# Performance work log

Measured on AMD Instinct MI355X. Metric: run time of the kernel, lower is better.

Reference implementation:

```python
import jax, jax.numpy as jnp
import numpy as np

V, D, L, H, FF, B, S = 32000, 2048, 4, 16, 8192, 2, 2048
DH = D // H
PRUNE_LAYERS = (1, 2)   # layers with an attached pruning module
KEEP_RATIO = 0.5        # keep_ratio arg of forward_prefill_with_pruning


def _rms(x, w, eps=1e-6):
    return x * w * jax.lax.rsqrt(jnp.mean(x * x, -1, keepdims=True) + eps)


def _rope(x):
    # x: [B,H,s,DH]; position_ids = arange(s), recomputed after every pruning step
    s = x.shape[2]
    half = DH // 2
    inv = 1.0 / (10000.0 ** (jnp.arange(half, dtype=jnp.float32) / half))
    ang = jnp.arange(s, dtype=jnp.float32)[:, None] * inv  # [s, half]
    cos, sin = jnp.cos(ang), jnp.sin(ang)
    x1, x2 = x[..., :half], x[..., half:]
    return jnp.concatenate([x1 * cos - x2 * sin, x1 * sin + x2 * cos], -1)


def _block(h, mask, wq, wk, wv, wo, wg, wu, wd, ln1, ln2):
    b, s, _ = h.shape
    hn = _rms(h, ln1)
    q = _rope((hn @ wq).reshape(b, s, H, DH).transpose(0, 2, 1, 3))
    k = _rope((hn @ wk).reshape(b, s, H, DH).transpose(0, 2, 1, 3))
    v = (hn @ wv).reshape(b, s, H, DH).transpose(0, 2, 1, 3)
    att = jnp.einsum('bhqd,bhkd->bhqk', q, k) / np.float32(np.sqrt(DH))
    allowed = jnp.tril(jnp.ones((s, s), bool)) & (mask[:, None, None, :] > 0)
    att = jnp.where(allowed, att, jnp.float32(-1e9))
    o = jnp.einsum('bhqk,bhkd->bhqd', jax.nn.softmax(att, -1), v)
    h = h + o.transpose(0, 2, 1, 3).reshape(b, s, D) @ wo
    hn = _rms(h, ln2)
    h = h + (jax.nn.silu(hn @ wg) * (hn @ wu)) @ wd
    return h


def _forward(input_ids, attention_mask, embed, wq, wk, wv, wo, wg, wu, wd, ln1, ln2, lnf, lm_head, scorer):
    h = embed[input_ids]        # [B,S,D]
    mask = attention_mask
    for i in range(L):
        if i in PRUNE_LAYERS:
            pi = PRUNE_LAYERS.index(i)
            # pruning module: Linear(D->2); keep score = logits[..., 0]
            sc = jnp.einsum('bsd,cd->bsc', h, scorer[pi])[..., 0]
            kk = max(1, int(h.shape[1] * KEEP_RATIO))      # static under jit
            _, idx = jax.lax.top_k(sc, kk)
            idx = jnp.sort(idx, -1)                        # sorted kept indices
            h = jnp.take_along_axis(h, idx[..., None], axis=1)
            mask = jnp.take_along_axis(mask, idx, axis=1)
        h = _block(h, mask, wq[i], wk[i], wv[i], wo[i], wg[i], wu[i], wd[i], ln1[i], ln2[i])
    return _rms(h, lnf) @ lm_head   # logits [B, S_pruned, V]


def setup_inputs() -> dict:
    key = jax.random.key(0)
    ks = jax.random.split(key, 12)
    g = lambda k, shape: jax.random.normal(k, shape, jnp.float32) * 0.02
    return {
        'input_ids': jax.random.randint(ks[0], (B, S), 0, V, jnp.int32),
        'attention_mask': jnp.ones((B, S), jnp.int32),
        'embed': g(ks[1], (V, D)),
        'wq': g(ks[2], (L, D, D)),
        'wk': g(ks[3], (L, D, D)),
        'wv': g(ks[4], (L, D, D)),
        'wo': g(ks[5], (L, D, D)),
        'wg': g(ks[6], (L, D, FF)),
        'wu': g(ks[7], (L, D, FF)),
        'wd': g(ks[8], (L, FF, D)),
        'ln1': jnp.ones((L, D), jnp.float32),
        'ln2': jnp.ones((L, D), jnp.float32),
        'lnf': jnp.ones((D,), jnp.float32),
        'lm_head': g(ks[9], (D, V)),
        'scorer': g(ks[10], (len(PRUNE_LAYERS), 2, D)),
    }


def reference(input_ids, attention_mask, embed, wq, wk, wv, wo, wg, wu, wd, ln1, ln2, lnf, lm_head, scorer):
    return _forward(input_ids, attention_mask, embed, wq, wk, wv, wo, wg, wu, wd, ln1, ln2, lnf, lm_head, scorer)
```

## Files before the change

kernel.cpp:

```cpp
#include <hip/hip_runtime.h>
#include <math.h>


#define DD 2048
#define HH 16
#define DHH 128
#define FFF 8192
#define BBATCH 2
#define SSEQ 2048
#define VV 32000
#define LLAYERS 4

typedef float4 f4;
typedef __attribute__((ext_vector_type(8))) short short8;
typedef __attribute__((ext_vector_type(4))) float f32x4;
typedef unsigned short u16;

__device__ inline u16 bf16rne(float x) {
    unsigned u = __float_as_uint(x);
    unsigned r = (u + 0x7FFFu + ((u >> 16) & 1u)) >> 16;
    return (u16)r;
}
__device__ inline float bf16tof(u16 h) {
    return __uint_as_float(((unsigned)h) << 16);
}

__device__ __forceinline__ void gload16(const u16* g, u16* l) {
    __builtin_amdgcn_global_load_lds(
        (const __attribute__((address_space(1))) unsigned int*)g,
        (__attribute__((address_space(3))) unsigned int*)l, 16, 0, 0);
}

#define BARRIER() do { asm volatile("" ::: "memory"); \
    __builtin_amdgcn_s_barrier(); asm volatile("" ::: "memory"); } while (0)

__device__ __forceinline__ void xcd_swz(int& bx, int& by) {
    int gy = gridDim.y;
    int nwg = gridDim.x * gy;
    int orig = bx * gy + by;
    int q = nwg >> 3, r = nwg & 7;
    int xcd = orig & 7, loc = orig >> 3;
    int swz = (xcd < r ? xcd * (q + 1) : r * (q + 1) + (xcd - r) * q) + loc;
    bx = swz / gy;
    by = swz % gy;
}

__global__ void k_embed(const int* __restrict__ ids, const float* __restrict__ emb,
                        float* __restrict__ out) {
    int row = blockIdx.x;
    int id  = ids[row];
    const f4* src = (const f4*)(emb + (size_t)id * DD);
    f4*       dst = (f4*)(out + (size_t)row * DD);
    for (int i = threadIdx.x; i < DD / 4; i += blockDim.x) dst[i] = src[i];
}

__global__ void k_copy_int(const int* __restrict__ src, int* __restrict__ dst, int n) {
    int i = blockIdx.x * blockDim.x + threadIdx.x;
    if (i < n) dst[i] = src[i];
}

__global__ void k_addN(float* __restrict__ H, const float* __restrict__ P,
                       long len, int nparts) {
    long i = (long)blockIdx.x * 256 + threadIdx.x;
    if (i >= len / 4) return;
    f4 h = ((f4*)H)[i];
    for (int z = 0; z < nparts; z++) {
        f4 p = ((const f4*)(P + (size_t)z * len))[i];
        h.x += p.x; h.y += p.y; h.z += p.z; h.w += p.w;
    }
    ((f4*)H)[i] = h;
}

__global__ __launch_bounds__(256) void k_rmsnorm_cvt(const float* __restrict__ x,
                                                     const float* __restrict__ w,
                                                     u16* __restrict__ OH,
                                                     u16* __restrict__ OL) {
    int row = blockIdx.x;
    const float* xr = x + (size_t)row * DD;
    float ss = 0.f;
    for (int i = threadIdx.x; i < DD / 4; i += blockDim.x) {
        f4 v = ((const f4*)xr)[i];
        ss += v.x * v.x + v.y * v.y + v.z * v.z + v.w * v.w;
    }
    for (int o = 32; o > 0; o >>= 1) ss += __shfl_down(ss, o);
    __shared__ float red[4];
    int wid = threadIdx.x >> 6, lane = threadIdx.x & 63;
    if (lane == 0) red[wid] = ss;
    __syncthreads();
    float tot = red[0] + red[1] + red[2] + red[3];
    float inv = 1.0f / sqrtf(tot / (float)DD + 1e-6f);
    for (int i = threadIdx.x; i < DD / 4; i += blockDim.x) {
        f4 v = ((const f4*)xr)[i];
        f4 wv = ((const f4*)w)[i];
        float o[4];
        o[0] = v.x * wv.x * inv; o[1] = v.y * wv.y * inv;
        o[2] = v.z * wv.z * inv; o[3] = v.w * wv.w * inv;
        ushort4 hv, lv;
        u16* hp = (u16*)&hv; u16* lp = (u16*)&lv;
#pragma unroll
        for (int j = 0; j < 4; j++) {
            u16 h = bf16rne(o[j]);
            hp[j] = h;
            lp[j] = bf16rne(o[j] - bf16tof(h));
        }
        *(ushort4*)&OH[(size_t)row * DD + i * 4] = hv;
        *(ushort4*)&OL[(size_t)row * DD + i * 4] = lv;
    }
}

__global__ __launch_bounds__(256) void k_cvt_w(const float* __restrict__ W,
                                               u16* __restrict__ WtH,
                                               u16* __restrict__ WtL,
                                               int K, int N, int nc0, int dn0,
                                               int writeLo) {
    __shared__ float T[64][65];
    int tid = threadIdx.x;
    int n0g = nc0 + blockIdx.x * 64;
    int k0  = blockIdx.y * 64;
#pragma unroll
    for (int it = 0; it < 4; it++) {
        int r = it * 16 + (tid >> 4);
        int c4 = (tid & 15) * 4;
        f4 v = *(const f4*)(W + (size_t)(k0 + r) * N + n0g + c4);
        T[r][c4 + 0] = v.x; T[r][c4 + 1] = v.y;
        T[r][c4 + 2] = v.z; T[r][c4 + 3] = v.w;
    }
    __syncthreads();
    int nl = tid >> 2;
    int ks = (tid & 3) * 16;
    u16 hi[16], lo[16];
#pragma unroll
    for (int j = 0; j < 16; j++) {
        float v = T[ks + j][nl];
        u16 h = bf16rne(v);
        hi[j] = h;
        lo[j] = bf16rne(v - bf16tof(h));
    }
    size_t base = (size_t)(dn0 + blockIdx.x * 64 + nl) * K + k0 + ks;
    *(short8*)&WtH[base]     = *(short8*)&hi[0];
    *(short8*)&WtH[base + 8] = *(short8*)&hi[8];
    if (writeLo) {
        *(short8*)&WtL[base]     = *(short8*)&lo[0];
        *(short8*)&WtL[base + 8] = *(short8*)&lo[8];
    }
}

template <int PASSES, int RES, int DUAL>
__global__ __launch_bounds__(256, 2) void k_bgemm(const u16* __restrict__ AH,
                                                  const u16* __restrict__ AL,
                                                  const u16* __restrict__ B1H,
                                                  const u16* __restrict__ B1L,
                                                  const u16* __restrict__ B2H,
                                                  const u16* __restrict__ B2L,
                                                  const float* __restrict__ Rsrc,
                                                  float* __restrict__ C,
                                                  u16* __restrict__ OH,
                                                  u16* __restrict__ OL,
                                                  int M, int ldC, int K) {
    constexpr int NW = DUAL ? 2 : 1;
    __shared__ u16 As[128 * 32];
    __shared__ u16 Bs[NW][128 * 32];
    int tid = threadIdx.x;
    int bx = blockIdx.x, by = blockIdx.y;
    xcd_swz(bx, by);
    int m0 = by * 128, n0 = bx * 128;
    int lane = tid & 63, w = tid >> 6;
    int wm = w >> 1, wn = w & 1;
    int lr = lane & 15, lq = lane >> 4;
    int grow = lane >> 2;
    int gcol = (lane & 3) * 8;

    f32x4 acc[NW][4][4];
#pragma unroll
    for (int u = 0; u < NW; u++)
#pragma unroll
        for (int i = 0; i < 4; i++)
#pragma unroll
            for (int j = 0; j < 4; j++)
#pragma unroll
                for (int r = 0; r < 4; r++) acc[u][i][j][r] = 0.f;

    const int KT = PASSES * K;
    for (int kb = 0; kb < KT; kb += 32) {
        int p  = (PASSES > 1) ? ((kb >= 2 * K) ? 2 : ((kb >= K) ? 1 : 0)) : 0;
        int ks = kb - p * K;
        const u16* Ab = ((p == 2) ? AL  : AH)  + (size_t)(m0 + w * 32) * K + ks;
        const u16* Bb = ((p == 1) ? B1L : B1H) + (size_t)(n0 + w * 32) * K + ks;
        __syncthreads();
        gload16(Ab + (size_t)grow * K + gcol,        &As[w * 1024]);
        gload16(Ab + (size_t)(grow + 16) * K + gcol, &As[w * 1024 + 512]);
        gload16(Bb + (size_t)grow * K + gcol,        &Bs[0][w * 1024]);
        gload16(Bb + (size_t)(grow + 16) * K + gcol, &Bs[0][w * 1024 + 512]);
        if constexpr (DUAL) {
            const u16* B2b = ((p == 1) ? B2L : B2H) + (size_t)(n0 + w * 32) * K + ks;
            gload16(B2b + (size_t)grow * K + gcol,        &Bs[1][w * 1024]);
            gload16(B2b + (size_t)(grow + 16) * K + gcol, &Bs[1][w * 1024 + 512]);
        }
        __syncthreads();
        short8 a[4];
#pragma unroll
        for (int i = 0; i < 4; i++)
            a[i] = *(const short8*)&As[(wm * 64 + i * 16 + lr) * 32 + lq * 8];
#pragma unroll
        for (int u = 0; u < NW; u++) {
#pragma unroll
            for (int j = 0; j < 4; j++) {
                short8 b = *(const short8*)&Bs[u][(wn * 64 + j * 16 + lr) * 32 + lq * 8];
#pragma unroll
                for (int i = 0; i < 4; i++)
                    acc[u][i][j] = __builtin_amdgcn_mfma_f32_16x16x32_bf16(
                        a[i], b, acc[u][i][j], 0, 0, 0);
            }
        }
    }
#pragma unroll
    for (int i = 0; i < 4; i++) {
#pragma unroll
        for (int j = 0; j < 4; j++) {
            int gm = m0 + wm * 64 + i * 16 + lq * 4;
            int gn = n0 + wn * 64 + j * 16 + lr;
#pragma unroll
            for (int r = 0; r < 4; r++) {
                size_t off = (size_t)(gm + r) * ldC + gn;
                if constexpr (DUAL) {
                    float g = acc[0][i][j][r], uu = acc[1][i][j][r];
                    float v = g / (1.0f + expf(-g)) * uu;
                    u16 h = bf16rne(v);
                    OH[off] = h;
                    OL[off] = bf16rne(v - bf16tof(h));
                } else {
                    float v = acc[0][i][j][r];
                    if constexpr (RES) v += Rsrc[off];
                    C[off] = v;
                }
            }
        }
    }
}

template <int MH>
__device__ __forceinline__ void loadA256(const u16* SMb, short8 (&aF)[4][2],
                                         int wm, int lr, int lq) {
    const u16* Ab = SMb + MH * 8192;
#pragma unroll
    for (int i = 0; i < 4; i++)
#pragma unroll
        for (int kk = 0; kk < 2; kk++)
            aF[i][kk] = *(const short8*)&Ab[(wm * 64 + i * 16 + lr) * 64 +
                                            (((kk * 4 + lq) ^ (lr & 7)) * 8)];
}

template <int MH, int NH>
__device__ __forceinline__ void quadB256(const u16* SMb, const short8 (&aF)[4][2],
                                         f32x4 (&acc)[8][4], int wn, int lr, int lq) {
    const u16* Bb = SMb + 16384 + NH * 8192;
    short8 bF[2][2];
#pragma unroll
    for (int j = 0; j < 2; j++)
#pragma unroll
        for (int kk = 0; kk < 2; kk++)
            bF[j][kk] = *(const short8*)&Bb[(wn * 32 + j * 16 + lr) * 64 +
                                            (((kk * 4 + lq) ^ (lr & 7)) * 8)];
    __builtin_amdgcn_s_setprio(1);
#pragma unroll
    for (int kk = 0; kk < 2; kk++)
#pragma unroll
        for (int j = 0; j < 2; j++)
#pragma unroll
            for (int i = 0; i < 4; i++)
                acc[MH * 4 + i][NH * 2 + j] = __builtin_amdgcn_mfma_f32_16x16x32_bf16(
                    aF[i][kk], bF[j][kk], acc[MH * 4 + i][NH * 2 + j], 0, 0, 0);
    __builtin_amdgcn_s_setprio(0);
}

template <int PASSES, int PLANE>
__global__ __launch_bounds__(512, 2) void k_bg256(const u16* __restrict__ AH,
                                                  const u16* __restrict__ AL,
                                                  const u16* __restrict__ BH,
                                                  const u16* __restrict__ BL,
                                                  float* __restrict__ C,
                                                  u16* __restrict__ OH,
                                                  u16* __restrict__ OL,
                                                  int M, int ldC, int K, int ld) {
    __shared__ u16 SM[65536];
    int tid = threadIdx.x;
    int bx = blockIdx.x, by = blockIdx.y;
    xcd_swz(bx, by);
    {
        size_t zo = (size_t)blockIdx.z * K;
        AH += zo; BH += zo;
        if constexpr (PASSES > 1) { AL += zo; BL += zo; }
        if constexpr (!PLANE) C += (size_t)blockIdx.z * ((size_t)M * ldC);
    }
    int m0 = by * 256, n0 = bx * 256;
    int w = tid >> 6, lane = tid & 63;
    int wm = w >> 2, wn = w & 3;
    int lr = lane & 15, lq = lane >> 4;

    f32x4 acc[8][4];
#pragma unroll
    for (int i = 0; i < 8; i++)
#pragma unroll
        for (int j = 0; j < 4; j++)
#pragma unroll
            for (int r = 0; r < 4; r++) acc[i][j][r] = 0.f;

    auto ASRC = [&](int T) -> const u16* {
        int kb = T * 64;
        if (PASSES > 1) {
            if (kb >= 2 * K) return AL + (kb - 2 * K);
            if (kb >= K)     return AH + (kb - K);
        }
        return AH + kb;
    };
    auto BSRC = [&](int T) -> const u16* {
        int kb = T * 64;
        if (PASSES > 1) {
            if (kb >= 2 * K) return BH + (kb - 2 * K);
            if (kb >= K)     return BL + (kb - K);
        }
        return BH + kb;
    };
    int srr = lane >> 3;
    int scc = ((lane & 7) ^ srr) * 8;
    auto STAGE_A = [&](int T, int h, int buf) {
        const u16* s = ASRC(T) + (size_t)(m0 + h * 128 + w * 16 + srr) * ld + scc;
        u16* d = SM + buf * 32768 + h * 8192 + w * 16 * 64;
        gload16(s, d);
        gload16(s + (size_t)8 * ld, d + 8 * 64);
    };
    auto STAGE_B = [&](int T, int h, int buf) {
        const u16* s = BSRC(T) + (size_t)(n0 + h * 128 + w * 16 + srr) * ld + scc;
        u16* d = SM + buf * 32768 + 16384 + h * 8192 + w * 16 * 64;
        gload16(s, d);
        gload16(s + (size_t)8 * ld, d + 8 * 64);
    };

    const int NT = (PASSES * K) >> 6;
    STAGE_A(0, 0, 0); STAGE_B(0, 0, 0);
    STAGE_A(0, 1, 0); STAGE_B(0, 1, 0);
    STAGE_A(1, 0, 1); STAGE_B(1, 0, 1);

    for (int T0 = 0; T0 < NT; T0 += 2) {
        int T1 = T0 + 1, T2 = T0 + 2, T3 = T0 + 3;
        short8 aF[4][2];
        STAGE_A(T1, 1, 1);
        asm volatile("s_waitcnt vmcnt(6)" ::: "memory");
        BARRIER();
        loadA256<0>(SM, aF, wm, lr, lq);
        quadB256<0, 0>(SM, aF, acc, wn, lr, lq);
        BARRIER();
        STAGE_B(T1, 1, 1);
        quadB256<0, 1>(SM, aF, acc, wn, lr, lq);
        BARRIER();
        if (T2 < NT) STAGE_A(T2, 0, 0);
        loadA256<1>(SM, aF, wm, lr, lq);
        quadB256<1, 0>(SM, aF, acc, wn, lr, lq);
        BARRIER();
        if (T2 < NT) STAGE_B(T2, 0, 0);
        quadB256<1, 1>(SM, aF, acc, wn, lr, lq);
        BARRIER();
        if (T2 < NT) {
            STAGE_A(T2, 1, 0);
            asm volatile("s_waitcnt vmcnt(6)" ::: "memory");
        } else {
            asm volatile("s_waitcnt vmcnt(0)" ::: "memory");
        }
        BARRIER();
        loadA256<0>(SM + 32768, aF, wm, lr, lq);
        quadB256<0, 0>(SM + 32768, aF, acc, wn, lr, lq);
        BARRIER();
        if (T2 < NT) STAGE_B(T2, 1, 0);
        quadB256<0, 1>(SM + 32768, aF, acc, wn, lr, lq);
        BARRIER();
        if (T3 < NT) STAGE_A(T3, 0, 1);
        loadA256<1>(SM + 32768, aF, wm, lr, lq);
        quadB256<1, 0>(SM + 32768, aF, acc, wn, lr, lq);
        BARRIER();
        if (T3 < NT) STAGE_B(T3, 0, 1);
        quadB256<1, 1>(SM + 32768, aF, acc, wn, lr, lq);
        BARRIER();
    }

#pragma unroll
    for (int i16 = 0; i16 < 8; i16++) {
#pragma unroll
        for (int jj = 0; jj < 4; jj++) {
            int gm = m0 + (i16 >> 2) * 128 + wm * 64 + (i16 & 3) * 16 + lq * 4;
            int gn = n0 + (jj >> 1) * 128 + wn * 32 + (jj & 1) * 16 + lr;
#pragma unroll
            for (int r = 0; r < 4; r++) {
                size_t off = (size_t)(gm + r) * ldC + gn;
                float v = acc[i16][jj][r];
                if constexpr (PLANE) {
                    u16 h = bf16rne(v);
                    OH[off] = h;
                    OL[off] = bf16rne(v - bf16tof(h));
                } else {
                    C[off] = v;
                }
            }
        }
    }
}

__global__ __launch_bounds__(256) void k_silu_cvt(const u16* __restrict__ Gh,
                                                  const u16* __restrict__ Gl,
                                                  u16* __restrict__ FH,
                                                  u16* __restrict__ FL, long n8) {
    long i = (long)blockIdx.x * 256 + threadIdx.x;
    if (i >= n8) return;
    short8 gh = ((const short8*)Gh)[i], gl = ((const short8*)Gl)[i];
    short8 uh = ((const short8*)FH)[i], ul = ((const short8*)FL)[i];
    short8 oh, ol;
#pragma unroll
    for (int e = 0; e < 8; e++) {
        float g = bf16tof((u16)gh[e]) + bf16tof((u16)gl[e]);
        float u = bf16tof((u16)uh[e]) + bf16tof((u16)ul[e]);
        float v = g / (1.0f + expf(-g)) * u;
        u16 h = bf16rne(v);
        oh[e] = (short)h;
        ol[e] = (short)bf16rne(v - bf16tof(h));
    }
    ((short8*)FH)[i] = oh;
    ((short8*)FL)[i] = ol;
}

__global__ void k_rope_table(float* __restrict__ cosT, float* __restrict__ sinT) {
    int idx = blockIdx.x * blockDim.x + threadIdx.x;
    if (idx >= SSEQ * 64) return;
    int pos = idx >> 6, d = idx & 63;
    float p   = (float)pow(10000.0, (double)d * (1.0 / 64.0));
    float inv = 1.0f / p;
    float ang = (float)pos * inv;
    cosT[idx] = (float)cos((double)ang);
    sinT[idx] = (float)sin((double)ang);
}

__global__ void k_rope(float* __restrict__ C,
                       const float* __restrict__ cosT, const float* __restrict__ sinT,
                       int s, int ld) {
    int bi = blockIdx.x;
    int h = bi % HH;
    int i = (bi / HH) % s;
    size_t base = (size_t)(bi / HH) * ld + h * DHH;
    int d = threadIdx.x;
    float c  = cosT[i * 64 + d];
    float sn = sinT[i * 64 + d];
    float x1 = C[base + d], x2 = C[base + 64 + d];
    C[base + d]      = x1 * c - x2 * sn;
    C[base + 64 + d] = x1 * sn + x2 * c;
    x1 = C[base + 2048 + d]; x2 = C[base + 2048 + 64 + d];
    C[base + 2048 + d]      = x1 * c - x2 * sn;
    C[base + 2048 + 64 + d] = x1 * sn + x2 * c;
}

__global__ __launch_bounds__(256) void k_cvt_qk(const float* __restrict__ C,
                                                u16* __restrict__ QHp, u16* __restrict__ QLp,
                                                u16* __restrict__ KHp, u16* __restrict__ KLp) {
    int row = blockIdx.x;
    int c = threadIdx.x * 8;
#pragma unroll
    for (int sec = 0; sec < 2; sec++) {
        const float* src = C + (size_t)row * 6144 + sec * 2048 + c;
        u16* dh = (sec ? KHp : QHp) + (size_t)row * 2048 + c;
        u16* dl = (sec ? KLp : QLp) + (size_t)row * 2048 + c;
        u16 hbuf[8], lbuf[8];
#pragma unroll
        for (int q = 0; q < 2; q++) {
            f4 v = *(const f4*)(src + q * 4);
            float a[4] = {v.x, v.y, v.z, v.w};
#pragma unroll
            for (int e = 0; e < 4; e++) {
                u16 h = bf16rne(a[e]);
                hbuf[q * 4 + e] = h;
                lbuf[q * 4 + e] = bf16rne(a[e] - bf16tof(h));
            }
        }
        *(short8*)dh = *(short8*)&hbuf[0];
        *(short8*)dl = *(short8*)&lbuf[0];
    }
}

__global__ __launch_bounds__(256) void k_cvt_vt(const float* __restrict__ C,
                                                u16* __restrict__ VtH,
                                                u16* __restrict__ VtL, int s) {
    __shared__ float T[64][132];
    int bh = blockIdx.y;
    int h = bh & 15, b = bh >> 4;
    int kv0 = blockIdx.x * 64;
    int t = threadIdx.x;
#pragma unroll
    for (int it = 0; it < 8; it++) {
        int kv = it * 8 + (t >> 5);
        int c4 = (t & 31) * 4;
        f4 v = *(const f4*)(C + (size_t)((size_t)b * s + kv0 + kv) * 6144 + 4096 + h * 128 + c4);
        T[kv][c4 + 0] = v.x; T[kv][c4 + 1] = v.y;
        T[kv][c4 + 2] = v.z; T[kv][c4 + 3] = v.w;
    }
    __syncthreads();
    int d = t >> 1, seg = t & 1;
    size_t base = ((size_t)bh * 128 + d) * s + kv0 + seg * 32;
#pragma unroll
    for (int g = 0; g < 4; g++) {
        u16 h8[8], l8[8];
#pragma unroll
        for (int e = 0; e < 8; e++) {
            float v = T[seg * 32 + g * 8 + e][d];
            u16 hh = bf16rne(v);
            h8[e] = hh;
            l8[e] = bf16rne(v - bf16tof(hh));
        }
        int gp = (g ^ ((d >> 1) & 3)) * 8;
        *(short8*)&VtH[base + gp] = *(short8*)&h8[0];
        *(short8*)&VtL[base + gp] = *(short8*)&l8[0];
    }
}

template <int PASSES>
__global__ __launch_bounds__(256, 2) void k_attn_mfma(
        const u16* __restrict__ QHp, const u16* __restrict__ QLp,
        const u16* __restrict__ KHp, const u16* __restrict__ KLp,
        const u16* __restrict__ VtH, const u16* __restrict__ VtL,
        const int* __restrict__ mask,
        u16* __restrict__ OH, u16* __restrict__ OL, int s) {
    constexpr int BUFU = (PASSES > 1) ? 16384 : 8192;
    constexpr int VOFF = (PASSES > 1) ? 8192 : 4096;
    __shared__ u16 SM[2 * BUFU + 5120];
    int tid = threadIdx.x, lane = tid & 63, w = tid >> 6;
    int lr = lane & 15, lq = lane >> 4;
    int grow = lane >> 2;
    int sgcol = (((lane & 3) ^ ((lane >> 3) & 3))) * 8;
    int gcol  = (lane & 3) * 8;
    int rc = (lq ^ ((lr >> 1) & 3)) * 8;
    int gx = gridDim.x;
    int NB = gx * gridDim.y;
    int orig = blockIdx.y * gx + blockIdx.x;
    int qq = NB >> 3, rr = NB & 7;
    int xcd = orig & 7, loc = orig >> 3;
    int swz = (xcd < rr ? xcd * (qq + 1) : rr * (qq + 1) + (xcd - rr) * qq) + loc;
    int bh = swz / gx;
    int qt = gx - 1 - (swz % gx);
    int h = bh & 15, b = bh >> 4;
    int q0 = qt * 128;
    size_t rb = (size_t)b * s;
    const u16* vtH = VtH + (size_t)bh * 128 * s;
    const u16* vtL = VtL + (size_t)bh * 128 * s;
    u16* PHw = SM + 2 * BUFU + w * 1280;
    u16* PLw = PHw + 640;
    const float scale = 0.08838834764831845f;

    short8 qh[2][4], ql[2][4];
#pragma unroll
    for (int st = 0; st < 2; st++) {
        const u16* qp = QHp + (rb + q0 + st * 64) * 2048 + h * 128 + w * 32;
#pragma unroll
        for (int it = 0; it < 4; it++)
            gload16(qp + (size_t)(it * 16 + grow) * 2048 + sgcol, SM + w * 2048 + it * 512);
        __syncthreads();
#pragma unroll
        for (int ks = 0; ks < 4; ks++)
            qh[st][ks] = *(const short8*)&SM[ks * 2048 + (w * 16 + lr) * 32 + rc];
        if constexpr (PASSES > 1) {
            __syncthreads();
            const u16* qp2 = QLp + (rb + q0 + st * 64) * 2048 + h * 128 + w * 32;
#pragma unroll
            for (int it = 0; it < 4; it++)
                gload16(qp2 + (size_t)(it * 16 + grow) * 2048 + sgcol, SM + w * 2048 + it * 512);
            __syncthreads();
#pragma unroll
            for (int ks = 0; ks < 4; ks++)
                ql[st][ks] = *(const short8*)&SM[ks * 2048 + (w * 16 + lr) * 32 + rc];
        }
        __syncthreads();
    }

    auto kv_stage = [&](int t, int buf) {
        u16* base = SM + buf * BUFU;
        const u16* kp = KHp + (rb + t * 32) * 2048 + h * 128 + w * 32;
        gload16(kp + (size_t)grow * 2048 + sgcol,        base + w * 1024);
        gload16(kp + (size_t)(16 + grow) * 2048 + sgcol, base + w * 1024 + 512);
        const u16* vp = vtH + (size_t)(w * 32) * s + t * 32;
        gload16(vp + (size_t)grow * s + gcol,        base + VOFF + (w * 32) * 32);
        gload16(vp + (size_t)(16 + grow) * s + gcol, base + VOFF + (w * 32 + 16) * 32);
        if constexpr (PASSES > 1) {
            const u16* kp2 = KLp + (rb + t * 32) * 2048 + h * 128 + w * 32;
            gload16(kp2 + (size_t)grow * 2048 + sgcol,        base + 4096 + w * 1024);
            gload16(kp2 + (size_t)(16 + grow) * 2048 + sgcol, base + 4096 + w * 1024 + 512);
            const u16* vp2 = vtL + (size_t)(w * 32) * s + t * 32;
            gload16(vp2 + (size_t)grow * s + gcol,        base + 12288 + (w * 32) * 32);
            gload16(vp2 + (size_t)(16 + grow) * s + gcol, base + 12288 + (w * 32 + 16) * 32);
        }
    };

    f32x4 o_acc[2][8];
#pragma unroll
    for (int st = 0; st < 2; st++)
#pragma unroll
        for (int j = 0; j < 8; j++)
#pragma unroll
            for (int r = 0; r < 4; r++) o_acc[st][j][r] = 0.f;
    float m_run[2][4], l_run[2][4];
#pragma unroll
    for (int st = 0; st < 2; st++)
#pragma unroll
        for (int r = 0; r < 4; r++) { m_run[st][r] = -3.0e38f; l_run[st][r] = 0.f; }

    int nt = (q0 + 128) >> 5;
    int mv0 = mask[rb + lr];
    int mv1 = mask[rb + 16 + lr];
    kv_stage(0, 0);
    for (int t = 0; t < nt; t++) {
        int bsel = t & 1;
        if (t + 1 < nt) {
            kv_stage(t + 1, 1 - bsel);
            if constexpr (PASSES > 1)
                asm volatile("s_waitcnt vmcnt(8)" ::: "memory");
            else
                asm volatile("s_waitcnt vmcnt(4)" ::: "memory");
        } else {
            asm volatile("s_waitcnt vmcnt(0)" ::: "memory");
        }
        BARRIER();
        int nmv0 = mv0, nmv1 = mv1;
        if (t + 1 < nt) {
            nmv0 = mask[rb + (t + 1) * 32 + lr];
            nmv1 = mask[rb + (t + 1) * 32 + 16 + lr];
        }
        const u16* KsH = SM + bsel * BUFU;
        const u16* KsL = KsH + 4096;
        const u16* VsH = SM + bsel * BUFU + VOFF;
        const u16* VsL = SM + bsel * BUFU + 12288;
#pragma unroll
        for (int st = 0; st < 2; st++) {
            if (t * 32 > q0 + st * 64 + w * 16 + 15) continue;
            f32x4 sa[2];
#pragma unroll
            for (int j = 0; j < 2; j++)
#pragma unroll
                for (int r = 0; r < 4; r++) sa[j][r] = 0.f;
#pragma unroll
            for (int j = 0; j < 2; j++) {
#pragma unroll
                for (int ks = 0; ks < 4; ks++) {
                    short8 kb = *(const short8*)&KsH[ks * 1024 + (j * 16 + lr) * 32 + rc];
                    sa[j] = __builtin_amdgcn_mfma_f32_16x16x32_bf16(qh[st][ks], kb, sa[j], 0, 0, 0);
                    if constexpr (PASSES > 1) {
                        short8 kl2 = *(const short8*)&KsL[ks * 1024 + (j * 16 + lr) * 32 + rc];
                        sa[j] = __builtin_amdgcn_mfma_f32_16x16x32_bf16(qh[st][ks], kl2, sa[j], 0, 0, 0);
                        sa[j] = __builtin_amdgcn_mfma_f32_16x16x32_bf16(ql[st][ks], kb, sa[j], 0, 0, 0);
                    }
                }
            }
            float sclv[4];
#pragma unroll
            for (int r = 0; r < 4; r++) {
                int ig = q0 + st * 64 + w * 16 + lq * 4 + r;
                float v0 = (t * 32 + lr <= ig && mv0 > 0) ? sa[0][r] * scale : -1.0e9f;
                float v1 = (t * 32 + 16 + lr <= ig && mv1 > 0) ? sa[1][r] * scale : -1.0e9f;
                float mx = fmaxf(v0, v1);
                mx = fmaxf(mx, __shfl_xor(mx, 1));
                mx = fmaxf(mx, __shfl_xor(mx, 2));
                mx = fmaxf(mx, __shfl_xor(mx, 4));
                mx = fmaxf(mx, __shfl_xor(mx, 8));
                float mo = m_run[st][r];
                float mn = fmaxf(mo, mx);
                float p0 = expf(v0 - mn), p1 = expf(v1 - mn);
                float ps = p0 + p1;
                ps += __shfl_xor(ps, 1);
                ps += __shfl_xor(ps, 2);
                ps += __shfl_xor(ps, 4);
                ps += __shfl_xor(ps, 8);
                sclv[r] = expf(mo - mn);
                m_run[st][r] = mn;
                l_run[st][r] = l_run[st][r] * sclv[r] + ps;
                int prow = lq * 4 + r;
                u16 h0 = bf16rne(p0);
                u16 h1 = bf16rne(p1);
                PHw[prow * 40 + lr] = h0;
                PHw[prow * 40 + 16 + lr] = h1;
                if constexpr (PASSES > 1) {
                    PLw[prow * 40 + lr] = bf16rne(p0 - bf16tof(h0));
                    PLw[prow * 40 + 16 + lr] = bf16rne(p1 - bf16tof(h1));
                }
            }
#pragma unroll
            for (int j = 0; j < 8; j++)
#pragma unroll
                for (int r = 0; r < 4; r++) o_acc[st][j][r] *= sclv[r];
            short8 ph = *(const short8*)&PHw[lr * 40 + lq * 8];
            short8 pl;
            if constexpr (PASSES > 1) pl = *(const short8*)&PLw[lr * 40 + lq * 8];
#pragma unroll
            for (int j = 0; j < 8; j++) {
                int vrow = j * 16 + lr;
                short8 vh = *(const short8*)&VsH[vrow * 32 + rc];
                o_acc[st][j] = __builtin_amdgcn_mfma_f32_16x16x32_bf16(ph, vh, o_acc[st][j], 0, 0, 0);
                if constexpr (PASSES > 1) {
                    short8 vl = *(const short8*)&VsL[vrow * 32 + rc];
                    o_acc[st][j] = __builtin_amdgcn_mfma_f32_16x16x32_bf16(ph, vl, o_acc[st][j], 0, 0, 0);
                    o_acc[st][j] = __builtin_amdgcn_mfma_f32_16x16x32_bf16(pl, vh, o_acc[st][j], 0, 0, 0);
                }
            }
        }
        BARRIER();
        mv0 = nmv0; mv1 = nmv1;
    }
#pragma unroll
    for (int st = 0; st < 2; st++) {
#pragma unroll
        for (int r = 0; r < 4; r++) {
            float linv = 1.0f / l_run[st][r];
            size_t rowoff = (rb + q0 + st * 64 + w * 16 + lq * 4 + r) * 2048 + h * 128 + lr;
#pragma unroll
            for (int j = 0; j < 8; j++) {
                float v = o_acc[st][j][r] * linv;
                u16 hh = bf16rne(v);
                OH[rowoff + j * 16] = hh;
                OL[rowoff + j * 16] = bf16rne(v - bf16tof(hh));
            }
        }
    }
}

__global__ __launch_bounds__(256, 2) void k_attn_f32(const float* __restrict__ Q,
                                                     const float* __restrict__ K,
                                                     const float* __restrict__ V,
                                                     const int* __restrict__ mask,
                                                     u16* __restrict__ OH,
                                                     u16* __restrict__ OL, int s, int ld) {
    int qt = blockIdx.x, bh = blockIdx.y;
    int h = bh & (HH - 1), b = bh >> 4;
    __shared__ float Qs[64][132];
    __shared__ float Ks[32 * 128];
    __shared__ float Vs[32][132];
    __shared__ float Ps[64][36];
    __shared__ float mrow[64], lrow[64];
    int tid = threadIdx.x;
    int tx = tid & 15, ty = tid >> 4;

#pragma unroll
    for (int p = 0; p < 2; p++) {
        int r = p * 32 + (tid >> 3);
        int kb = (tid & 7) * 4;
        const float* src = Q + (size_t)(b * s + qt * 64 + r) * ld + h * DHH;
#pragma unroll
        for (int q = 0; q < 4; q++)
            *(f4*)&Qs[r][kb + 32 * q] = *(const f4*)(src + kb + 32 * q);
    }
    if (tid < 64) { mrow[tid] = -3.0e38f; lrow[tid] = 0.f; }

    float acc[4][8];
#pragma unroll
    for (int i = 0; i < 4; i++)
#pragma unroll
        for (int c = 0; c < 8; c++) acc[i][c] = 0.f;
    const float scale = 0.08838834764831845f;

    int ktmax = 2 * (qt + 1);
    for (int kt = 0; kt < ktmax; kt++) {
        __syncthreads();
#pragma unroll
        for (int p = 0; p < 4; p++) {
            int c = p * 8 + (tid >> 5);
            int kk = (tid & 31) * 4;
            size_t g = (size_t)(b * s + kt * 32 + c) * ld + h * DHH + kk;
            f4 kv = *(const f4*)(K + g);
            int ch = (kk >> 2) ^ (c >> 1);
            *(f4*)&Ks[c * 128 + ch * 4] = kv;
            *(f4*)&Vs[c][kk] = *(const f4*)(V + g);
        }
        __syncthreads();
        float sv[4][2];
#pragma unroll
        for (int i = 0; i < 4; i++) { sv[i][0] = 0.f; sv[i][1] = 0.f; }
        for (int kk = 0; kk < 128; kk += 4) {
            f4 qv[4];
#pragma unroll
            for (int i = 0; i < 4; i++) qv[i] = *(const f4*)&Qs[ty * 4 + i][kk];
#pragma unroll
            for (int j = 0; j < 2; j++) {
                int c = tx * 2 + j;
                int ch = (kk >> 2) ^ (c >> 1);
                f4 kv = *(const f4*)&Ks[c * 128 + ch * 4];
#pragma unroll
                for (int i = 0; i < 4; i++)
                    sv[i][j] += qv[i].x * kv.x + qv[i].y * kv.y +
                                qv[i].z * kv.z + qv[i].w * kv.w;
            }
        }
        float scl[4];
#pragma unroll
        for (int i = 0; i < 4; i++) {
            int r = ty * 4 + i;
            int igl = qt * 64 + r;
#pragma unroll
            for (int j = 0; j < 2; j++) {
                int jg = kt * 32 + tx * 2 + j;
                bool ok = (jg <= igl) && (mask[b * s + jg] > 0);
                sv[i][j] = ok ? sv[i][j] * scale : -1.0e9f;
            }
            float rmax = fmaxf(sv[i][0], sv[i][1]);
            rmax = fmaxf(rmax, __shfl_xor(rmax, 1));
            rmax = fmaxf(rmax, __shfl_xor(rmax, 2));
            rmax = fmaxf(rmax, __shfl_xor(rmax, 4));
            rmax = fmaxf(rmax, __shfl_xor(rmax, 8));
            float mold = mrow[r];
            float mnew = fmaxf(mold, rmax);
            float p0 = expf(sv[i][0] - mnew);
            float p1 = expf(sv[i][1] - mnew);
            float ps = p0 + p1;
            ps += __shfl_xor(ps, 1);
            ps += __shfl_xor(ps, 2);
            ps += __shfl_xor(ps, 4);
            ps += __shfl_xor(ps, 8);
            scl[i] = expf(mold - mnew);
            if (tx == 0) { mrow[r] = mnew; lrow[r] = lrow[r] * scl[i] + ps; }
            float2 pw; pw.x = p0; pw.y = p1;
            *(float2*)&Ps[r][tx * 2] = pw;
        }
        __syncthreads();
#pragma unroll
        for (int i = 0; i < 4; i++) {
            float sc = scl[i];
#pragma unroll
            for (int c = 0; c < 8; c++) acc[i][c] *= sc;
        }
        for (int jj = 0; jj < 32; jj += 4) {
            f4 pv[4];
#pragma unroll
            for (int i = 0; i < 4; i++) pv[i] = *(const f4*)&Ps[ty * 4 + i][jj];
#pragma unroll
            for (int j2 = 0; j2 < 4; j2++) {
                f4 va = *(const f4*)&Vs[jj + j2][tx * 4];
                f4 vb = *(const f4*)&Vs[jj + j2][64 + tx * 4];
#pragma unroll
                for (int i = 0; i < 4; i++) {
                    float p = (&pv[i].x)[j2];
                    acc[i][0] += p * va.x; acc[i][1] += p * va.y;
                    acc[i][2] += p * va.z; acc[i][3] += p * va.w;
                    acc[i][4] += p * vb.x; acc[i][5] += p * vb.y;
                    acc[i][6] += p * vb.z; acc[i][7] += p * vb.w;
                }
            }
        }
    }
    __syncthreads();
#pragma unroll
    for (int i = 0; i < 4; i++) {
        int r = ty * 4 + i;
        float linv = 1.0f / lrow[r];
        size_t ob = (size_t)(b * s + qt * 64 + r) * DD + h * DHH;
        ushort4 h1, l1, h2, l2;
        u16 *h1p = (u16*)&h1, *l1p = (u16*)&l1, *h2p = (u16*)&h2, *l2p = (u16*)&l2;
#pragma unroll
        for (int c = 0; c < 4; c++) {
            float v = acc[i][c] * linv;
            u16 hh = bf16rne(v);
            h1p[c] = hh; l1p[c] = bf16rne(v - bf16tof(hh));
            float v2 = acc[i][c + 4] * linv;
            u16 hh2 = bf16rne(v2);
            h2p[c] = hh2; l2p[c] = bf16rne(v2 - bf16tof(hh2));
        }
        *(ushort4*)&OH[ob + tx * 4] = h1;
        *(ushort4*)&OL[ob + tx * 4] = l1;
        *(ushort4*)&OH[ob + 64 + tx * 4] = h2;
        *(ushort4*)&OL[ob + 64 + tx * 4] = l2;
    }
}

__global__ __launch_bounds__(256) void k_score(const float* __restrict__ Hb,
                                               const float* __restrict__ srow,
                                               float* __restrict__ sc) {
    int row = blockIdx.x;
    const float* xr = Hb + (size_t)row * DD;
    float ss = 0.f;
    for (int i = threadIdx.x; i < DD / 4; i += blockDim.x) {
        f4 a = ((const f4*)xr)[i];
        f4 w = ((const f4*)srow)[i];
        ss += a.x * w.x + a.y * w.y + a.z * w.z + a.w * w.w;
    }
    for (int o = 32; o > 0; o >>= 1) ss += __shfl_down(ss, o);
    __shared__ float red[4];
    int wid = threadIdx.x >> 6, lane = threadIdx.x & 63;
    if (lane == 0) red[wid] = ss;
    __syncthreads();
    if (threadIdx.x == 0) sc[row] = red[0] + red[1] + red[2] + red[3];
}

__global__ __launch_bounds__(256) void k_rank(const float* __restrict__ sc,
                                              int* __restrict__ flg, int s, int kk) {
    int b = blockIdx.x / s, i = blockIdx.x % s;
    const float* scb = sc + (size_t)b * s;
    float vi = scb[i];
    int cnt = 0;
    for (int j = threadIdx.x; j < s; j += 256) {
        float vj = scb[j];
        if (vj > vi || (vj == vi && j < i)) cnt++;
    }
    for (int o = 32; o > 0; o >>= 1) cnt += __shfl_down(cnt, o);
    __shared__ int red[4];
    int wid = threadIdx.x >> 6, lane = threadIdx.x & 63;
    if (lane == 0) red[wid] = cnt;
    __syncthreads();
    if (threadIdx.x == 0) flg[b * s + i] = ((red[0] + red[1] + red[2] + red[3]) < kk) ? 1 : 0;
}

__global__ void k_compact(const int* __restrict__ flg, int* __restrict__ idx, int s, int kk) {
    int b = blockIdx.x;
    if (threadIdx.x == 0) {
        int p = 0;
        for (int i = 0; i < s; i++)
            if (flg[b * s + i]) idx[b * kk + (p++)] = i;
    }
}

__global__ void k_gather(const float* __restrict__ Hin, const int* __restrict__ idx,
                         float* __restrict__ Hout, int s, int kk) {
    int row = blockIdx.x;
    int b = row / kk, p = row % kk;
    int i = idx[b * kk + p];
    const f4* src = (const f4*)(Hin + (size_t)(b * s + i) * DD);
    f4* dst = (f4*)(Hout + (size_t)row * DD);
    for (int t = threadIdx.x; t < DD / 4; t += blockDim.x) dst[t] = src[t];
}

__global__ void k_gather_mask(const int* __restrict__ Min, const int* __restrict__ idx,
                              int* __restrict__ Mout, int s, int kk) {
    int t = blockIdx.x * blockDim.x + threadIdx.x;
    if (t < BBATCH * kk) {
        int b = t / kk, p = t % kk;
        Mout[t] = Min[b * s + idx[b * kk + p]];
    }
}

extern "C" void kernel_launch(void* const* d_in, const int* in_sizes, int n_in,
                              void* d_out, int out_size, void* d_ws, size_t ws_size,
                              hipStream_t stream) {
    const int*   input_ids = (const int*)d_in[0];
    const int*   attn_mask = (const int*)d_in[1];
    const float* embed     = (const float*)d_in[2];
    const float* wq        = (const float*)d_in[3];
    const float* wk        = (const float*)d_in[4];
    const float* wv        = (const float*)d_in[5];
    const float* wo        = (const float*)d_in[6];
    const float* wg        = (const float*)d_in[7];
    const float* wu        = (const float*)d_in[8];
    const float* wd        = (const float*)d_in[9];
    const float* ln1       = (const float*)d_in[10];
    const float* ln2       = (const float*)d_in[11];
    const float* lnf       = (const float*)d_in[12];
    const float* lm_head   = (const float*)d_in[13];
    const float* scorer    = (const float*)d_in[14];

    float* ws = (float*)d_ws;
    const size_t R = (size_t)BBATCH * SSEQ * DD;
    const size_t MISC_FLOATS = 2 * SSEQ * 64 + 5 * (size_t)BBATCH * SSEQ + 1024;
    const size_t NEED_A = (14 * R + MISC_FLOATS) * 4;
    const bool bigws = (ws_size >= NEED_A);

    float* H0   = ws;
    float* H1   = ws + R;
    float* CQKV = ws + 2 * R;
    u16*   AH   = (u16*)(ws + 5 * R);
    u16*   AL   = AH + (size_t)4096 * DD;

    u16* QHp = (u16*)(ws + 6 * R);
    u16* QLp = QHp + (size_t)4096 * DD;
    u16* KHp = (u16*)(ws + 7 * R);
    u16* KLp = KHp + (size_t)4096 * DD;
    u16* VtH = (u16*)(ws + 8 * R);
    u16* VtL = VtH + (size_t)4096 * DD;
    u16* FH  = (u16*)(ws + 6 * R);
    u16* FL  = (u16*)(ws + 8 * R);
    u16* WH1 = (u16*)(ws + 10 * R);
    u16* WL1 = WH1 + (size_t)FFF * DD;
    u16* WH2 = (u16*)(ws + 12 * R);
    u16* WL2 = WH2 + (size_t)FFF * DD;
    u16* WDH = (u16*)(ws + 10 * R);
    u16* WDL = WDH + (size_t)DD * FFF;
    u16* WQKVH = (u16*)(ws + 10 * R);
    u16* WQKVL = WQKVH + (size_t)6144 * DD;

    u16* cWgH = (u16*)CQKV;
    u16* cWgL = cWgH + (size_t)2048 * DD;
    u16* cWuH = cWgL + (size_t)2048 * DD;
    u16* cWuL = cWuH + (size_t)2048 * DD;
    u16* cFH  = (u16*)(ws + 3 * R);
    u16* cFL  = cFH + (size_t)4096 * 2048;
    u16* cWdH = (u16*)(ws + 4 * R);
    u16* cWdL = cWdH + (size_t)2048 * DD;

    float* miscB = ws + (bigws ? 14 * R : 6 * R);
    float* COS = miscB;
    float* SIN = COS + SSEQ * 64;
    float* SC  = SIN + SSEQ * 64;
    int*   FLG = (int*)(SC + (size_t)BBATCH * SSEQ);
    int*   IDX = FLG + BBATCH * SSEQ;
    int*   M0  = IDX + BBATCH * SSEQ;
    int*   M1  = M0 + BBATCH * SSEQ;

    k_rope_table<<<(SSEQ * 64 + 255) / 256, 256, 0, stream>>>(COS, SIN);
    k_embed<<<BBATCH * SSEQ, 256, 0, stream>>>(input_ids, embed, H0);
    k_copy_int<<<(BBATCH * SSEQ + 255) / 256, 256, 0, stream>>>(attn_mask, M0, BBATCH * SSEQ);

    float* Hc = H0; float* Nc = H1;
    int*   Mc = M0; int*   Mt = M1;
    int s = SSEQ;

    for (int l = 0; l < LLAYERS; l++) {
        if (l == 1 || l == 2) {
            int pi = l - 1;
            int kk = s / 2;
            k_score<<<BBATCH * s, 256, 0, stream>>>(Hc, scorer + (size_t)pi * 2 * DD, SC);
            k_rank<<<BBATCH * s, 256, 0, stream>>>(SC, FLG, s, kk);
            k_compact<<<BBATCH, 64, 0, stream>>>(FLG, IDX, s, kk);
            k_gather<<<BBATCH * kk, 256, 0, stream>>>(Hc, IDX, Nc, s, kk);
            k_gather_mask<<<(BBATCH * kk + 255) / 256, 256, 0, stream>>>(Mc, IDX, Mt, s, kk);
            { float* t = Hc; Hc = Nc; Nc = t; }
            { int* t = Mc; Mc = Mt; Mt = t; }
            s = kk;
        }
        int rows = BBATCH * s;
        const bool hiP = (l < 2);
        const int wlo = hiP ? 1 : 0;
        const float* Wq = wq + (size_t)l * DD * DD;
        const float* Wk = wk + (size_t)l * DD * DD;
        const float* Wv = wv + (size_t)l * DD * DD;
        const float* Wo = wo + (size_t)l * DD * DD;
        const float* Wg = wg + (size_t)l * DD * FFF;
        const float* Wu = wu + (size_t)l * DD * FFF;
        const float* Wd = wd + (size_t)l * FFF * DD;
        const float* L1 = ln1 + (size_t)l * DD;
        const float* L2 = ln2 + (size_t)l * DD;

        dim3 gWd(DD / 64, DD / 64);

        k_rmsnorm_cvt<<<rows, 256, 0, stream>>>(Hc, L1, AH, AL);
        if (bigws) {
            k_cvt_w<<<gWd, 256, 0, stream>>>(Wq, WQKVH, WQKVL, DD, DD, 0, 0, wlo);
            k_cvt_w<<<gWd, 256, 0, stream>>>(Wk, WQKVH, WQKVL, DD, DD, 0, 2048, wlo);
            k_cvt_w<<<gWd, 256, 0, stream>>>(Wv, WQKVH, WQKVL, DD, DD, 0, 4096, wlo);
            if (rows >= 2048) {
                dim3 gQKV(6144 / 256, rows / 256);
                if (hiP) k_bg256<3,0><<<gQKV,512,0,stream>>>(AH,AL,WQKVH,WQKVL,CQKV,nullptr,nullptr,rows,6144,DD,DD);
                else     k_bg256<1,0><<<gQKV,512,0,stream>>>(AH,AL,WQKVH,WQKVL,CQKV,nullptr,nullptr,rows,6144,DD,DD);
            } else {
                dim3 gQKV(6144 / 128, rows / 128);
                k_bgemm<1,0,0><<<gQKV,256,0,stream>>>(AH,AL,WQKVH,WQKVL,nullptr,nullptr,nullptr,CQKV,nullptr,nullptr,rows,6144,DD);
            }
        } else {
            u16* WtH = (u16*)Nc;
            u16* WtL = WtH + (size_t)DD * DD;
            dim3 gG(DD / 128, rows / 128);
            const float* Wqkv[3] = {Wq, Wk, Wv};
            for (int q3 = 0; q3 < 3; q3++) {
                k_cvt_w<<<gWd, 256, 0, stream>>>(Wqkv[q3], WtH, WtL, DD, DD, 0, 0, wlo);
                float* Cb = CQKV + q3 * 2048;
                if (hiP) k_bgemm<3,0,0><<<gG,256,0,stream>>>(AH,AL,WtH,WtL,nullptr,nullptr,nullptr,Cb,nullptr,nullptr,rows,6144,DD);
                else     k_bgemm<1,0,0><<<gG,256,0,stream>>>(AH,AL,WtH,WtL,nullptr,nullptr,nullptr,Cb,nullptr,nullptr,rows,6144,DD);
            }
        }
        k_rope<<<rows * HH, 64, 0, stream>>>(CQKV, COS, SIN, s, 6144);

        if (bigws) {
            k_cvt_qk<<<rows, 256, 0, stream>>>(CQKV, QHp, QLp, KHp, KLp);
            k_cvt_vt<<<dim3(s / 64, BBATCH * HH), 256, 0, stream>>>(CQKV, VtH, VtL, s);
            if (hiP) k_attn_mfma<3><<<dim3(s / 128, BBATCH * HH), 256, 0, stream>>>(
                         QHp, QLp, KHp, KLp, VtH, VtL, Mc, AH, AL, s);
            else     k_attn_mfma<1><<<dim3(s / 128, BBATCH * HH), 256, 0, stream>>>(
                         QHp, QLp, KHp, KLp, VtH, VtL, Mc, AH, AL, s);
        } else {
            k_attn_f32<<<dim3(s / 64, BBATCH * HH), 256, 0, stream>>>(
                CQKV, CQKV + 2048, CQKV + 4096, Mc, AH, AL, s, 6144);
        }

        {
            u16* WtH = bigws ? WQKVH : (u16*)Nc;
            u16* WtL = bigws ? (WQKVH + (size_t)DD * DD) : ((u16*)Nc + (size_t)DD * DD);
            k_cvt_w<<<gWd, 256, 0, stream>>>(Wo, WtH, WtL, DD, DD, 0, 0, wlo);
            if (bigws && hiP) {
                int SK = (rows >= 4096) ? 2 : 4;
                float* P = ws + 2 * R;
                dim3 g(DD / 256, rows / 256, SK);
                k_bg256<3,0><<<g, 512, 0, stream>>>(AH, AL, WtH, WtL, P,
                                                    nullptr, nullptr, rows, DD, DD / SK, DD);
                long len = (long)rows * DD;
                k_addN<<<(len / 4 + 255) / 256, 256, 0, stream>>>(Hc, P, len, SK);
            } else {
                dim3 gG(DD / 128, rows / 128);
                if (hiP) k_bgemm<3,1,0><<<gG,256,0,stream>>>(AH,AL,WtH,WtL,nullptr,nullptr,Hc,Hc,nullptr,nullptr,rows,DD,DD);
                else     k_bgemm<1,1,0><<<gG,256,0,stream>>>(AH,AL,WtH,WtL,nullptr,nullptr,Hc,Hc,nullptr,nullptr,rows,DD,DD);
            }
        }

        k_rmsnorm_cvt<<<rows, 256, 0, stream>>>(Hc, L2, AH, AL);
        if (bigws && rows >= 2048) {
            k_cvt_w<<<dim3(FFF / 64, DD / 64), 256, 0, stream>>>(Wg, WH1, WL1, DD, FFF, 0, 0, wlo);
            k_cvt_w<<<dim3(FFF / 64, DD / 64), 256, 0, stream>>>(Wu, WH2, WL2, DD, FFF, 0, 0, wlo);
            u16* Gh = (l == 0) ? (u16*)(ws + R) : (u16*)(ws + 2 * R);
            u16* Gl = (u16*)(ws + 3 * R);
            dim3 gMLP(FFF / 256, rows / 256);
            if (hiP) {
                k_bg256<3,1><<<gMLP,512,0,stream>>>(AH,AL,WH1,WL1,nullptr,Gh,Gl,rows,FFF,DD,DD);
                k_bg256<3,1><<<gMLP,512,0,stream>>>(AH,AL,WH2,WL2,nullptr,FH,FL,rows,FFF,DD,DD);
            } else {
                k_bg256<1,1><<<gMLP,512,0,stream>>>(AH,AL,WH1,WL1,nullptr,Gh,Gl,rows,FFF,DD,DD);
                k_bg256<1,1><<<gMLP,512,0,stream>>>(AH,AL,WH2,WL2,nullptr,FH,FL,rows,FFF,DD,DD);
            }
            long n8 = (long)rows * FFF / 8;
            k_silu_cvt<<<(n8 + 255) / 256, 256, 0, stream>>>(Gh, Gl, FH, FL, n8);
            k_cvt_w<<<dim3(DD / 64, FFF / 64), 256, 0, stream>>>(Wd, WDH, WDL, FFF, DD, 0, 0, wlo);
            int SK = (rows >= 4096) ? 2 : 4;
            float* P = ws + 2 * R;
            dim3 gD(DD / 256, rows / 256, SK);
            if (hiP) k_bg256<3,0><<<gD,512,0,stream>>>(FH,FL,WDH,WDL,P,nullptr,nullptr,rows,DD,FFF/SK,FFF);
            else     k_bg256<1,0><<<gD,512,0,stream>>>(FH,FL,WDH,WDL,P,nullptr,nullptr,rows,DD,FFF/SK,FFF);
            long len = (long)rows * DD;
            k_addN<<<(len / 4 + 255) / 256, 256, 0, stream>>>(Hc, P, len, SK);
        } else if (bigws) {
            k_cvt_w<<<dim3(FFF / 64, DD / 64), 256, 0, stream>>>(Wg, WH1, WL1, DD, FFF, 0, 0, wlo);
            k_cvt_w<<<dim3(FFF / 64, DD / 64), 256, 0, stream>>>(Wu, WH2, WL2, DD, FFF, 0, 0, wlo);
            k_bgemm<1,0,1><<<dim3(FFF/128, rows/128),256,0,stream>>>(AH,AL,WH1,WL1,WH2,WL2,nullptr,nullptr,FH,FL,rows,FFF,DD);
            k_cvt_w<<<dim3(DD / 64, FFF / 64), 256, 0, stream>>>(Wd, WDH, WDL, FFF, DD, 0, 0, wlo);
            k_bgemm<1,1,0><<<dim3(DD/128, rows/128),256,0,stream>>>(FH,FL,WDH,WDL,nullptr,nullptr,Hc,Hc,nullptr,nullptr,rows,DD,FFF);
        } else {
            for (int ffc = 0; ffc < FFF; ffc += 2048) {
                k_cvt_w<<<dim3(2048 / 64, DD / 64), 256, 0, stream>>>(Wg, cWgH, cWgL, DD, FFF, ffc, 0, wlo);
                k_cvt_w<<<dim3(2048 / 64, DD / 64), 256, 0, stream>>>(Wu, cWuH, cWuL, DD, FFF, ffc, 0, wlo);
                if (hiP) k_bgemm<3,0,1><<<dim3(16, rows/128),256,0,stream>>>(AH,AL,cWgH,cWgL,cWuH,cWuL,nullptr,nullptr,cFH,cFL,rows,2048,DD);
                else     k_bgemm<1,0,1><<<dim3(16, rows/128),256,0,stream>>>(AH,AL,cWgH,cWgL,cWuH,cWuL,nullptr,nullptr,cFH,cFL,rows,2048,DD);
                k_cvt_w<<<dim3(DD / 64, 2048 / 64), 256, 0, stream>>>(Wd + (size_t)ffc * DD, cWdH, cWdL, 2048, DD, 0, 0, wlo);
                if (hiP) k_bgemm<3,1,0><<<dim3(DD/128, rows/128),256,0,stream>>>(cFH,cFL,cWdH,cWdL,nullptr,nullptr,Hc,Hc,nullptr,nullptr,rows,DD,2048);
                else     k_bgemm<1,1,0><<<dim3(DD/128, rows/128),256,0,stream>>>(cFH,cFL,cWdH,cWdL,nullptr,nullptr,Hc,Hc,nullptr,nullptr,rows,DD,2048);
            }
        }
    }

    int rows = BBATCH * s;
    u16* AHf = (u16*)Nc;
    u16* ALf = AHf + (size_t)rows * DD;
    u16* LmH = bigws ? (u16*)(ws + 6 * R) : (u16*)CQKV;
    k_rmsnorm_cvt<<<rows, 256, 0, stream>>>(Hc, lnf, AHf, ALf);
    k_cvt_w<<<dim3(VV / 64, DD / 64), 256, 0, stream>>>(lm_head, LmH, LmH, DD, VV, 0, 0, 0);
    if (bigws) {
        k_bg256<1, 0><<<dim3(VV / 256, rows / 256), 512, 0, stream>>>(
            AHf, ALf, LmH, LmH, (float*)d_out, nullptr, nullptr, rows, VV, DD, DD);
    } else {
        k_bgemm<1,0,0><<<dim3(VV / 128, rows / 128), 256, 0, stream>>>(
            AHf, ALf, LmH, LmH, nullptr, nullptr, nullptr, (float*)d_out,
            nullptr, nullptr, rows, VV, DD);
    }
}
```

Measured before the change: 4.773 ms.

## Restructure 256-tile GEMM main loop into simple double-buffered single-barrier pipeline

Replaces the fine-grained interleaved staging schedule, which had many barriers per K-tile and half-tile loads, with a plain double buffer. Each iteration issues the whole next tile's global-to-LDS loads, reads all A and B fragments for the current tile into registers, and runs all 32 MFMAs. It then waits for the loads to finish and hits one barrier. This cuts barrier count and scheduling complexity, but keeps more fragments live in registers and exposes load latency at the end of each iteration with a vmcnt(0) wait.

```diff
diff --git a/kernel.cpp b/kernel.cpp
--- a/kernel.cpp
+++ b/kernel.cpp
@@ -238,41 +238,6 @@
     }
 }
 
-template <int MH>
-__device__ __forceinline__ void loadA256(const u16* SMb, short8 (&aF)[4][2],
-                                         int wm, int lr, int lq) {
-    const u16* Ab = SMb + MH * 8192;
-#pragma unroll
-    for (int i = 0; i < 4; i++)
-#pragma unroll
-        for (int kk = 0; kk < 2; kk++)
-            aF[i][kk] = *(const short8*)&Ab[(wm * 64 + i * 16 + lr) * 64 +
-                                            (((kk * 4 + lq) ^ (lr & 7)) * 8)];
-}
-
-template <int MH, int NH>
-__device__ __forceinline__ void quadB256(const u16* SMb, const short8 (&aF)[4][2],
-                                         f32x4 (&acc)[8][4], int wn, int lr, int lq) {
-    const u16* Bb = SMb + 16384 + NH * 8192;
-    short8 bF[2][2];
-#pragma unroll
-    for (int j = 0; j < 2; j++)
-#pragma unroll
-        for (int kk = 0; kk < 2; kk++)
-            bF[j][kk] = *(const short8*)&Bb[(wn * 32 + j * 16 + lr) * 64 +
-                                            (((kk * 4 + lq) ^ (lr & 7)) * 8)];
-    __builtin_amdgcn_s_setprio(1);
-#pragma unroll
-    for (int kk = 0; kk < 2; kk++)
-#pragma unroll
-        for (int j = 0; j < 2; j++)
-#pragma unroll
-            for (int i = 0; i < 4; i++)
-                acc[MH * 4 + i][NH * 2 + j] = __builtin_amdgcn_mfma_f32_16x16x32_bf16(
-                    aF[i][kk], bF[j][kk], acc[MH * 4 + i][NH * 2 + j], 0, 0, 0);
-    __builtin_amdgcn_s_setprio(0);
-}
-
 template <int PASSES, int PLANE>
 __global__ __launch_bounds__(512, 2) void k_bg256(const u16* __restrict__ AH,
                                                   const u16* __restrict__ AL,
@@ -335,51 +300,79 @@
         gload16(s, d);
         gload16(s + (size_t)8 * ld, d + 8 * 64);
     };
+    auto RD_A = [&](const u16* SMb, int MH, short8 (&aF)[4][2]) {
+        const u16* Ab = SMb + MH * 8192;
+#pragma unroll
+        for (int i = 0; i < 4; i++)
+#pragma unroll
+            for (int kk = 0; kk < 2; kk++)
+                aF[i][kk] = *(const short8*)&Ab[(wm * 64 + i * 16 + lr) * 64 +
+                                                (((kk * 4 + lq) ^ (lr & 7)) * 8)];
+    };
+    auto RD_B = [&](const u16* SMb, int NH, short8 (&bF)[2][2]) {
+        const u16* Bb = SMb + 16384 + NH * 8192;
+#pragma unroll
+        for (int j = 0; j < 2; j++)
+#pragma unroll
+            for (int kk = 0; kk < 2; kk++)
+                bF[j][kk] = *(const short8*)&Bb[(wn * 32 + j * 16 + lr) * 64 +
+                                                (((kk * 4 + lq) ^ (lr & 7)) * 8)];
+    };
 
     const int NT = (PASSES * K) >> 6;
     STAGE_A(0, 0, 0); STAGE_B(0, 0, 0);
     STAGE_A(0, 1, 0); STAGE_B(0, 1, 0);
-    STAGE_A(1, 0, 1); STAGE_B(1, 0, 1);
-
-    for (int T0 = 0; T0 < NT; T0 += 2) {
-        int T1 = T0 + 1, T2 = T0 + 2, T3 = T0 + 3;
-        short8 aF[4][2];
-        STAGE_A(T1, 1, 1);
-        asm volatile("s_waitcnt vmcnt(6)" ::: "memory");
-        BARRIER();
-        loadA256<0>(SM, aF, wm, lr, lq);
-        quadB256<0, 0>(SM, aF, acc, wn, lr, lq);
-        BARRIER();
-        STAGE_B(T1, 1, 1);
-        quadB256<0, 1>(SM, aF, acc, wn, lr, lq);
-        BARRIER();
-        if (T2 < NT) STAGE_A(T2, 0, 0);
-        loadA256<1>(SM, aF, wm, lr, lq);
-        quadB256<1, 0>(SM, aF, acc, wn, lr, lq);
-        BARRIER();
-        if (T2 < NT) STAGE_B(T2, 0, 0);
-        quadB256<1, 1>(SM, aF, acc, wn, lr, lq);
-        BARRIER();
-        if (T2 < NT) {
-            STAGE_A(T2, 1, 0);
-            asm volatile("s_waitcnt vmcnt(6)" ::: "memory");
-        } else {
+    asm volatile("s_waitcnt vmcnt(0)" ::: "memory");
+    BARRIER();
+
+    for (int T = 0; T < NT; T++) {
+        int cur = T & 1;
+        const u16* SMb = SM + cur * 32768;
+        short8 a0[4][2], a1[4][2], b0[2][2], b1[2][2];
+        if (T + 1 < NT) { STAGE_A(T + 1, 0, cur ^ 1); STAGE_B(T + 1, 0, cur ^ 1); }
+        RD_A(SMb, 0, a0);
+        RD_B(SMb, 0, b0);
+        if (T + 1 < NT) { STAGE_A(T + 1, 1, cur ^ 1); STAGE_B(T + 1, 1, cur ^ 1); }
+        RD_B(SMb, 1, b1);
+        RD_A(SMb, 1, a1);
+        __builtin_amdgcn_s_setprio(1);
+#pragma unroll
+        for (int kk = 0; kk < 2; kk++)
+#pragma unroll
+            for (int j = 0; j < 2; j++)
+#pragma unroll
+                for (int i = 0; i < 4; i++)
+                    acc[i][j] = __builtin_amdgcn_mfma_f32_16x16x32_bf16(
+                        a0[i][kk], b0[j][kk], acc[i][j], 0, 0, 0);
+#pragma unroll
+        for (int kk = 0; kk < 2; kk++)
+#pragma unroll
+            for (int j = 0; j < 2; j++)
+#pragma unroll
+                for (int i = 0; i < 4; i++)
+                    acc[i][2 + j] = __builtin_amdgcn_mfma_f32_16x16x32_bf16(
+                        a0[i][kk], b1[j][kk], acc[i][2 + j], 0, 0, 0);
+#pragma unroll
+        for (int kk = 0; kk < 2; kk++)
+#pragma unroll
+            for (int j = 0; j < 2; j++)
+#pragma unroll
+                for (int i = 0; i < 4; i++)
+                    acc[4 + i][j] = __builtin_amdgcn_mfma_f32_16x16x32_bf16(
+                        a1[i][kk], b0[j][kk], acc[4 + i][j], 0, 0, 0);
+#pragma unroll
+        for (int kk = 0; kk < 2; kk++)
+#pragma unroll
+            for (int j = 0; j < 2; j++)
+#pragma unroll
+                for (int i = 0; i < 4; i++)
+                    acc[4 + i][2 + j] = __builtin_amdgcn_mfma_f32_16x16x32_bf16(
+                        a1[i][kk], b1[j][kk], acc[4 + i][2 + j], 0, 0, 0);
+        __builtin_amdgcn_s_setprio(0);
+        if (T + 1 < NT) {
             asm volatile("s_waitcnt vmcnt(0)" ::: "memory");
-        }
-        BARRIER();
-        loadA256<0>(SM + 32768, aF, wm, lr, lq);
-        quadB256<0, 0>(SM + 32768, aF, acc, wn, lr, lq);
-        BARRIER();
-        if (T2 < NT) STAGE_B(T2, 1, 0);
-        quadB256<0, 1>(SM + 32768, aF, acc, wn, lr, lq);
-        BARRIER();
-        if (T3 < NT) STAGE_A(T3, 0, 1);
-        loadA256<1>(SM + 32768, aF, wm, lr, lq);
-        quadB256<1, 0>(SM + 32768, aF, acc, wn, lr, lq);
-        BARRIER();
-        if (T3 < NT) STAGE_B(T3, 0, 1);
-        quadB256<1, 1>(SM + 32768, aF, acc, wn, lr, lq);
-        BARRIER();
+            BARRIER();
+        }
     }
 
 #pragma unroll
```

Result: faster. 4.593 ms (-3.8%).
